# Performance work log

Measured on AMD Instinct MI355X. Metric: run time of the kernel, lower is better.

Reference implementation:

```python
import jax, jax.numpy as jnp
import numpy as np

TEMP = 0.07
BASE_TEMP = 0.07
BANK = 8192
B = 512      # samples per view; features has 2*B rows
D = 128      # feature dim
N_CLASSES = 100


def _l2norm(x, axis=-1):
    return x / jnp.linalg.norm(x, axis=axis, keepdims=True)


def setup_inputs() -> dict:
    key = jax.random.key(0)
    k1, k2, k3, k4, k5 = jax.random.split(key, 5)
    # SupCon features are L2-normalized embeddings; two views stacked: [2B, 1, D]
    features = _l2norm(jax.random.normal(k1, (2 * B, 1, D), jnp.float32))
    label = jax.random.randint(k2, (B,), 0, N_CLASSES)
    # memory banks stored as [D, bank_size] (lightly MemoryBankModule layout)
    bank1 = _l2norm(jax.random.normal(k3, (D, BANK), jnp.float32), axis=0)
    bank2 = _l2norm(jax.random.normal(k4, (D, BANK), jnp.float32), axis=0)
    bank_labels = jax.random.randint(k5, (BANK,), 0, N_CLASSES)
    return {"features": features, "label": label, "bank1": bank1,
            "bank2": bank2, "bank_labels": bank_labels}


def _branch_loss(cf, pos_mask, neg_mask):
    # cf: [N, D] anchor==contrast features
    logits = jnp.matmul(cf, cf.T) / TEMP                       # [N, N]
    logits = logits - jax.lax.stop_gradient(logits.max(axis=1, keepdims=True))
    # denominator: sum of exp(logits) over NEGATIVES only (square(mask-1) mask)
    denom = jnp.log((jnp.exp(logits) * neg_mask).sum(axis=1, keepdims=True))
    log_prob = logits - denom                                  # [N, N]
    mean_log_prob_pos = (pos_mask * log_prob).sum(axis=1) / pos_mask.sum(axis=1)
    return -(TEMP / BASE_TEMP) * mean_log_prob_pos             # [N]


def reference(features, label, bank1, bank2, bank_labels):
    d = features.shape[-1]
    fr = features.reshape(-1, d)                # [2B, D]
    nb = fr.shape[0] // 2
    f1, f2 = fr[:nb], fr[nb:]                   # [B, D] each

    labels_all = jnp.concatenate([bank_labels.reshape(-1, 1),
                                  label.reshape(-1, 1)], axis=0)   # [N, 1]
    same = (labels_all == labels_all.T)                            # [N, N]
    mask = same.astype(fr.dtype)
    n = mask.shape[0]
    self_mask = 1.0 - jnp.eye(n, dtype=fr.dtype)
    pos_mask = mask * self_mask                 # positives excluding self
    neg_mask = jnp.square(mask - 1.0)           # 1 where labels differ

    cf1 = jnp.concatenate([bank2.T, f1], axis=0)   # [N, D]
    cf2 = jnp.concatenate([bank1.T, f2], axis=0)   # [N, D]

    class_loss = (_branch_loss(cf1, pos_mask, neg_mask)
                  + _branch_loss(cf2, pos_mask, neg_mask)) / 2.0
    loss = class_loss.mean()
    return (loss, loss, loss)
```

## Files before the change

### kernel.cpp

```cpp
#include <hip/hip_runtime.h>
#include <math.h>

#define NTOT 8704
#define BANKN 8192
#define NB 512
#define DIM 128
#define INVT (1.0f / 0.07f)
#define C2L 20.6099131801f
#define NCHUNK 17
#define TPC 8
#define BN 64

using short8 = __attribute__((ext_vector_type(8))) short;
using ushort8 = __attribute__((ext_vector_type(8))) unsigned short;
using f32x4 = __attribute__((ext_vector_type(4))) float;

static __device__ __forceinline__ ushort f2bf(float f) {
  union { float f; unsigned u; } v;
  v.f = f;
  unsigned r = v.u + 0x7fffu + ((v.u >> 16) & 1u);
  return (ushort)(r >> 16);
}

static __device__ __forceinline__ float fast_exp2(float x) {
#if __has_builtin(__builtin_amdgcn_exp2f)
  return __builtin_amdgcn_exp2f(x);
#else
  return exp2f(x);
#endif
}

__global__ __launch_bounds__(1024) void prep_kernel(
    const int* __restrict__ bank_labels, const int* __restrict__ label,
    int* __restrict__ inv, int* __restrict__ lo, int* __restrict__ hi) {
  __shared__ int h[16][100];
  __shared__ int st[101];
  __shared__ int sc[128];
  const int tid = threadIdx.x;
  const int w = tid >> 6;
  for (int i = tid; i < 1600; i += 1024) (&h[0][0])[i] = 0;
  __syncthreads();
  for (int i = tid; i < NTOT; i += 1024) {
    const int v = (i < BANKN) ? bank_labels[i] : label[i - BANKN];
    atomicAdd(&h[w][v], 1);
  }
  __syncthreads();
  int tot = 0;
  if (tid < 128) {
    if (tid < 100) {
#pragma unroll
      for (int w2 = 0; w2 < 16; ++w2) tot += h[w2][tid];
    }
    sc[tid] = tot;
  }
  __syncthreads();
#pragma unroll
  for (int off = 1; off < 128; off <<= 1) {
    int add = 0;
    if (tid < 128 && tid >= off) add = sc[tid - off];
    __syncthreads();
    if (tid < 128) sc[tid] += add;
    __syncthreads();
  }
  if (tid < 100) {
    st[tid] = sc[tid] - tot;
    if (tid == 99) st[100] = sc[99];
  }
  __syncthreads();
  if (tid < 100) {
    int base = st[tid];
#pragma unroll
    for (int w2 = 0; w2 < 16; ++w2) {
      const int t = h[w2][tid];
      h[w2][tid] = base;
      base += t;
    }
  }
  __syncthreads();
  for (int i = tid; i < NTOT; i += 1024) {
    const int v = (i < BANKN) ? bank_labels[i] : label[i - BANKN];
    const int p = atomicAdd(&h[w][v], 1);
    inv[i] = p;
    lo[p] = st[v];
    hi[p] = st[v + 1];
  }
}

__global__ void pack_kernel(const float* __restrict__ features,
                            const float* __restrict__ bank1,
                            const float* __restrict__ bank2,
                            const int* __restrict__ inv,
                            ushort* __restrict__ cf1b,
                            ushort* __restrict__ cf2b,
                            float* __restrict__ zp) {
  const int branch = blockIdx.z;
  ushort* __restrict__ dst = branch ? cf2b : cf1b;
  const int tx = threadIdx.x, ty = threadIdx.y;
  const int bx = blockIdx.x, by = blockIdx.y;
  const int tid = ty * 32 + tx;
  {
    const int bid = (blockIdx.z * gridDim.y + blockIdx.y) * gridDim.x + bx;
    const int gid = bid * 256 + tid;
    if (gid < NTOT)
      reinterpret_cast<float4*>(zp)[gid] = make_float4(0.f, 0.f, 0.f, 0.f);
  }
  if (bx < 256) {
    const float* __restrict__ src = branch ? bank1 : bank2;
    __shared__ float tile[32][33];
    const int col = bx * 32 + tx;
#pragma unroll
    for (int s = 0; s < 32; s += 8)
      tile[ty + s][tx] = src[(size_t)(by * 32 + ty + s) * BANKN + col];
    __syncthreads();
    const int k = by * 32 + tx;
#pragma unroll
    for (int s = 0; s < 32; s += 8) {
      const int p = inv[bx * 32 + ty + s];
      dst[(size_t)p * DIM + k] = f2bf(tile[tx][ty + s]);
    }
  } else {
#pragma unroll
    for (int s = 0; s < 32; s += 8) {
      const int jr = (bx - 256) * 32 + ty + s;
      const int k = by * 32 + tx;
      const float v = features[(size_t)(branch * NB + jr) * DIM + k];
      const int p = inv[BANKN + jr];
      dst[(size_t)p * DIM + k] = f2bf(v);
    }
  }
}

__global__ __launch_bounds__(256) void supcon_mfma_kernel(
    const ushort* __restrict__ cf1b, const ushort* __restrict__ cf2b,
    const int* __restrict__ lo, const int* __restrict__ hi,
    float* __restrict__ zp) {
  const int rb = blockIdx.x;
  const int chunk = blockIdx.y;
  const int branch = blockIdx.z;
  const ushort* __restrict__ cf = branch ? cf2b : cf1b;

  const int tid = threadIdx.x;
  const int wid = tid >> 6, lane = tid & 63;
  const int l15 = lane & 15, l4 = lane >> 4;
  const int rowW = rb * 128 + wid * 32;

  __shared__ ushort Bt[3][BN * DIM];

  short8 a[2][4];
#pragma unroll
  for (int rt = 0; rt < 2; ++rt) {
    const int r = rowW + rt * 16 + l15;
#pragma unroll
    for (int ks = 0; ks < 4; ++ks)
      a[rt][ks] = *reinterpret_cast<const short8*>(cf + (size_t)r * DIM + ks * 32 + l4 * 8);
  }
  int rlo[2][4], rhi[2][4];
#pragma unroll
  for (int rt = 0; rt < 2; ++rt)
#pragma unroll
    for (int rg = 0; rg < 4; ++rg) {
      const int rr = rowW + rt * 16 + l4 * 4 + rg;
      rlo[rt][rg] = lo[rr];
      rhi[rt][rg] = hi[rr];
    }
  const int u_lo = lo[rowW];
  const int u_hi = hi[rowW + 31];
  const int lo_last = lo[rowW + 31];
  const int hi_first = hi[rowW];

  float Zr[2][4] = {};
  float Pr[2][4] = {};

  auto STAGE = [&](int t, int buf) {
    const int col0 = (chunk * TPC + t) * BN;
#pragma unroll
    for (int it = 0; it < 4; ++it) {
      const int o = it * 256 + tid;
      const int row = o >> 4, cc = o & 15;
      const ushort* src =
          cf + (size_t)(col0 + row) * DIM + ((cc ^ (row & 15)) * 8);
      ushort* dst = &Bt[buf][(it * 256 + wid * 64) * 8];
      __builtin_amdgcn_global_load_lds(
          (const __attribute__((address_space(1))) void*)src,
          (__attribute__((address_space(3))) void*)dst, 16, 0, 0);
    }
  };

  STAGE(0, 0);
  STAGE(1, 1);

  for (int t = 0; t < TPC; ++t) {
    if (t + 1 < TPC)
      asm volatile("s_waitcnt vmcnt(4)" ::: "memory");
    else
      asm volatile("s_waitcnt vmcnt(0)" ::: "memory");
    __builtin_amdgcn_s_barrier();
    if (t + 2 < TPC) STAGE(t + 2, (t + 2) % 3);

    const int col0 = (chunk * TPC + t) * BN;
    const ushort* __restrict__ B = &Bt[t % 3][0];

    f32x4 acc[2][4];
#pragma unroll
    for (int rt = 0; rt < 2; ++rt)
#pragma unroll
      for (int ct = 0; ct < 4; ++ct) acc[rt][ct] = (f32x4){0.f, 0.f, 0.f, 0.f};

#pragma unroll
    for (int ks = 0; ks < 4; ++ks) {
      short8 b[4];
#pragma unroll
      for (int ct = 0; ct < 4; ++ct) {
        const int r = ct * 16 + l15;
        const int swz = (ks * 4 + l4) ^ (r & 15);
        b[ct] = *reinterpret_cast<const short8*>(&B[r * DIM + swz * 8]);
      }
#pragma unroll
      for (int rt = 0; rt < 2; ++rt)
#pragma unroll
        for (int ct = 0; ct < 4; ++ct)
          acc[rt][ct] = __builtin_amdgcn_mfma_f32_16x16x32_bf16(
              a[rt][ks], b[ct], acc[rt][ct], 0, 0, 0);
    }

    if (col0 + BN <= u_lo || col0 >= u_hi) {
#pragma unroll
      for (int ct = 0; ct < 4; ++ct)
#pragma unroll
        for (int rt = 0; rt < 2; ++rt)
#pragma unroll
          for (int rg = 0; rg < 4; ++rg)
            Zr[rt][rg] += fast_exp2(fmaf(acc[rt][ct][rg], C2L, -C2L));
    } else if (col0 >= lo_last && col0 + BN <= hi_first) {
#pragma unroll
      for (int ct = 0; ct < 4; ++ct)
#pragma unroll
        for (int rt = 0; rt < 2; ++rt)
#pragma unroll
          for (int rg = 0; rg < 4; ++rg) Pr[rt][rg] += acc[rt][ct][rg];
    } else {
#pragma unroll
      for (int ct = 0; ct < 4; ++ct) {
        const int c = col0 + ct * 16 + l15;
#pragma unroll
        for (int rt = 0; rt < 2; ++rt)
#pragma unroll
          for (int rg = 0; rg < 4; ++rg) {
            const float v = acc[rt][ct][rg];
            const float e = fast_exp2(fmaf(v, C2L, -C2L));
            const bool s = (c >= rlo[rt][rg]) && (c < rhi[rt][rg]);
            Zr[rt][rg] += s ? 0.0f : e;
            Pr[rt][rg] += s ? v : 0.0f;
          }
      }
    }
  }

  float* Zrow = zp;
  float* Prow = zp + 2 * NTOT;
#pragma unroll
  for (int rt = 0; rt < 2; ++rt)
#pragma unroll
    for (int rg = 0; rg < 4; ++rg) {
      float z = Zr[rt][rg], p = Pr[rt][rg];
#pragma unroll
      for (int off = 1; off < 16; off <<= 1) {
        z += __shfl_xor(z, off);
        p += __shfl_xor(p, off);
      }
      if (l15 == 0) {
        const int row = rowW + rt * 16 + l4 * 4 + rg;
        atomicAdd(&Zrow[branch * NTOT + row], z);
        atomicAdd(&Prow[branch * NTOT + row], p);
      }
    }
}

__global__ __launch_bounds__(1024) void loss_kernel(const float* __restrict__ zp,
                                                    const int* __restrict__ lo,
                                                    const int* __restrict__ hi,
                                                    float* __restrict__ out) {
  const int tid = threadIdx.x;
  const float* Zrow = zp;
  const float* Prow = zp + 2 * NTOT;
  float local = 0.f;
  for (int idx = tid; idx < 2 * NTOT; idx += 1024) {
    const int row = (idx >= NTOT) ? idx - NTOT : idx;
    const float z = Zrow[idx];
    const float p = Prow[idx];
    const float C = (float)(hi[row] - lo[row] - 1);
    const float denom = INVT + logf(z);
    local += -((INVT * (p - 1.0f)) / C - denom);
  }
  __shared__ float s[1024];
  s[tid] = local;
  __syncthreads();
  for (int st = 512; st > 0; st >>= 1) {
    if (tid < st) s[tid] += s[tid + st];
    __syncthreads();
  }
  if (tid == 0) {
    const float v = s[0] / (2.0f * NTOT);
    out[0] = v; out[1] = v; out[2] = v;
  }
}

extern "C" void kernel_launch(void* const* d_in, const int* in_sizes, int n_in,
                              void* d_out, int out_size, void* d_ws,
                              size_t ws_size, hipStream_t stream) {
  const float* features = (const float*)d_in[0];
  const int* label = (const int*)d_in[1];
  const float* bank1 = (const float*)d_in[2];
  const float* bank2 = (const float*)d_in[3];
  const int* bank_labels = (const int*)d_in[4];
  float* out = (float*)d_out;

  char* ws = (char*)d_ws;
  ushort* cf1b = (ushort*)(ws);
  ushort* cf2b = (ushort*)(ws + 2228224);
  int* inv = (int*)(ws + 4456448);
  int* lo = (int*)(ws + 4491264);
  int* hi = (int*)(ws + 4526080);
  float* zp = (float*)(ws + 4560896);

  prep_kernel<<<dim3(1), dim3(1024), 0, stream>>>(bank_labels, label, inv, lo,
                                                  hi);
  pack_kernel<<<dim3(272, DIM / 32, 2), dim3(32, 8), 0, stream>>>(
      features, bank1, bank2, inv, cf1b, cf2b, zp);
  supcon_mfma_kernel<<<dim3(NTOT / 128, NCHUNK, 2), dim3(256), 0, stream>>>(
      cf1b, cf2b, lo, hi, zp);
  loss_kernel<<<dim3(1), dim3(1024), 0, stream>>>(zp, lo, hi, out);
}
```

Baseline: 151.2 us.

## Split single-block label counting sort into three multi-block kernels

Replaces the single 1024-thread prep kernel, which histogrammed and scattered all 8704 labels in one block, with three kernels: a 34-block histogram using global atomics (which also zeroes the zp accumulator), a single-block prefix scan, and a 34-block scatter that uses global atomic cursors. The zp zeroing moves out of pack_kernel, and a memset clears the new count buffers. The goal is to spread the serial prep work across many CUs. The cost is two extra kernel launches plus a memset, and global atomic contention on only 100 counters.

```diff
diff --git a/kernel.cpp b/kernel.cpp
--- a/kernel.cpp
+++ b/kernel.cpp
@@ -30,60 +30,49 @@
 #endif
 }
 
-__global__ __launch_bounds__(1024) void prep_kernel(
-    const int* __restrict__ bank_labels, const int* __restrict__ label,
-    int* __restrict__ inv, int* __restrict__ lo, int* __restrict__ hi) {
-  __shared__ int h[16][100];
-  __shared__ int st[101];
+__global__ void prep1_kernel(const int* __restrict__ bank_labels,
+                             const int* __restrict__ label,
+                             int* __restrict__ cnt,
+                             float* __restrict__ zp) {
+  const int i = blockIdx.x * 256 + threadIdx.x;
+  reinterpret_cast<float4*>(zp)[i] = make_float4(0.f, 0.f, 0.f, 0.f);
+  const int v = (i < BANKN) ? bank_labels[i] : label[i - BANKN];
+  atomicAdd(&cnt[v], 1);
+}
+
+__global__ void prep2_kernel(const int* __restrict__ cnt,
+                             int* __restrict__ st, int* __restrict__ cur) {
   __shared__ int sc[128];
   const int tid = threadIdx.x;
-  const int w = tid >> 6;
-  for (int i = tid; i < 1600; i += 1024) (&h[0][0])[i] = 0;
+  int mine = (tid < 100) ? cnt[tid] : 0;
+  sc[tid] = mine;
   __syncthreads();
-  for (int i = tid; i < NTOT; i += 1024) {
-    const int v = (i < BANKN) ? bank_labels[i] : label[i - BANKN];
-    atomicAdd(&h[w][v], 1);
-  }
-  __syncthreads();
-  int tot = 0;
-  if (tid < 128) {
-    if (tid < 100) {
-#pragma unroll
-      for (int w2 = 0; w2 < 16; ++w2) tot += h[w2][tid];
-    }
-    sc[tid] = tot;
-  }
-  __syncthreads();
 #pragma unroll
   for (int off = 1; off < 128; off <<= 1) {
-    int add = 0;
-    if (tid < 128 && tid >= off) add = sc[tid - off];
+    int add = (tid >= off) ? sc[tid - off] : 0;
     __syncthreads();
-    if (tid < 128) sc[tid] += add;
+    sc[tid] += add;
     __syncthreads();
   }
   if (tid < 100) {
-    st[tid] = sc[tid] - tot;
+    const int ex = sc[tid] - mine;
+    st[tid] = ex;
+    cur[tid] = ex;
     if (tid == 99) st[100] = sc[99];
   }
-  __syncthreads();
-  if (tid < 100) {
-    int base = st[tid];
-#pragma unroll
-    for (int w2 = 0; w2 < 16; ++w2) {
-      const int t = h[w2][tid];
-      h[w2][tid] = base;
-      base += t;
-    }
-  }
-  __syncthreads();
-  for (int i = tid; i < NTOT; i += 1024) {
-    const int v = (i < BANKN) ? bank_labels[i] : label[i - BANKN];
-    const int p = atomicAdd(&h[w][v], 1);
-    inv[i] = p;
-    lo[p] = st[v];
-    hi[p] = st[v + 1];
-  }
+}
+
+__global__ void prep3_kernel(const int* __restrict__ bank_labels,
+                             const int* __restrict__ label,
+                             const int* __restrict__ st, int* __restrict__ cur,
+                             int* __restrict__ inv, int* __restrict__ lo,
+                             int* __restrict__ hi) {
+  const int i = blockIdx.x * 256 + threadIdx.x;
+  const int v = (i < BANKN) ? bank_labels[i] : label[i - BANKN];
+  const int p = atomicAdd(&cur[v], 1);
+  inv[i] = p;
+  lo[p] = st[v];
+  hi[p] = st[v + 1];
 }
 
 __global__ void pack_kernel(const float* __restrict__ features,
@@ -91,19 +80,11 @@
                             const float* __restrict__ bank2,
                             const int* __restrict__ inv,
                             ushort* __restrict__ cf1b,
-                            ushort* __restrict__ cf2b,
-                            float* __restrict__ zp) {
+                            ushort* __restrict__ cf2b) {
   const int branch = blockIdx.z;
   ushort* __restrict__ dst = branch ? cf2b : cf1b;
   const int tx = threadIdx.x, ty = threadIdx.y;
   const int bx = blockIdx.x, by = blockIdx.y;
-  const int tid = ty * 32 + tx;
-  {
-    const int bid = (blockIdx.z * gridDim.y + blockIdx.y) * gridDim.x + bx;
-    const int gid = bid * 256 + tid;
-    if (gid < NTOT)
-      reinterpret_cast<float4*>(zp)[gid] = make_float4(0.f, 0.f, 0.f, 0.f);
-  }
   if (bx < 256) {
     const float* __restrict__ src = branch ? bank1 : bank2;
     __shared__ float tile[32][33];
@@ -322,11 +303,19 @@
   int* lo = (int*)(ws + 4491264);
   int* hi = (int*)(ws + 4526080);
   float* zp = (float*)(ws + 4560896);
-
-  prep_kernel<<<dim3(1), dim3(1024), 0, stream>>>(bank_labels, label, inv, lo,
-                                                  hi);
+  int* cnt = (int*)(ws + 4700160);
+  int* st = (int*)(ws + 4700560);
+  int* cur = (int*)(ws + 4700964);
+
+  hipMemsetAsync(ws + 4700160, 0, 1204, stream);
+
+  prep1_kernel<<<dim3(34), dim3(256), 0, stream>>>(bank_labels, label, cnt,
+                                                   zp);
+  prep2_kernel<<<dim3(1), dim3(128), 0, stream>>>(cnt, st, cur);
+  prep3_kernel<<<dim3(34), dim3(256), 0, stream>>>(bank_labels, label, st, cur,
+                                                   inv, lo, hi);
   pack_kernel<<<dim3(272, DIM / 32, 2), dim3(32, 8), 0, stream>>>(
-      features, bank1, bank2, inv, cf1b, cf2b, zp);
+      features, bank1, bank2, inv, cf1b, cf2b);
   supcon_mfma_kernel<<<dim3(NTOT / 128, NCHUNK, 2), dim3(256), 0, stream>>>(
       cf1b, cf2b, lo, hi, zp);
   loss_kernel<<<dim3(1), dim3(1024), 0, stream>>>(zp, lo, hi, out);
```

Result: slower. 171.1 us (+13.2%).
